# Kernel optimization log

Measured on AMD Instinct MI355X. Metric: run time of the kernel, lower is better.

Reference implementation:

```python
import jax, jax.numpy as jnp
import numpy as np

B, N, C = 1, 768, 384
H, P = 12, 4
DP = 128  # dim_pair
HP3 = H * P * 3  # 144


def linear(x, W, b):
    # torch nn.Linear: y = x @ W.T + b, W shape (out, in)
    return jnp.einsum('...i,oi->...o', x, W) + b


def setup_inputs() -> dict:
    key = jax.random.key(0)
    ks = jax.random.split(key, 24)
    w = lambda k, *s: jax.random.normal(k, s, jnp.float32) * 0.02
    inp = {
        'single': jax.random.normal(ks[0], (B, N, C), jnp.float32),
        'pair': jax.random.normal(ks[1], (B, N, N, DP), jnp.float32),
        'rot': jax.random.normal(ks[2], (B, N, 3, 3), jnp.float32),
        'trans': jax.random.normal(ks[3], (B, N, 3), jnp.float32),
        'Wq': w(ks[4], C, C), 'bq': jnp.zeros((C,), jnp.float32),
        'Wk': w(ks[5], C, C), 'bk': jnp.zeros((C,), jnp.float32),
        'Wv': w(ks[6], C, C), 'bv': jnp.zeros((C,), jnp.float32),
        'Wpb': w(ks[7], H, DP), 'bpb': jnp.zeros((H,), jnp.float32),
        'Wqp': w(ks[8], HP3, C), 'bqp': jnp.zeros((HP3,), jnp.float32),
        'Wkp': w(ks[9], HP3, C), 'bkp': jnp.zeros((HP3,), jnp.float32),
        'Wvp': w(ks[10], HP3, C), 'bvp': jnp.zeros((HP3,), jnp.float32),
        'Wo': w(ks[11], C, C), 'bo': jnp.zeros((C,), jnp.float32),
        'Wpo': w(ks[12], C, HP3), 'bpo': jnp.zeros((C,), jnp.float32),
        'ln_w': jnp.ones((C,), jnp.float32), 'ln_b': jnp.zeros((C,), jnp.float32),
    }
    return inp


def reference(single, pair, rot, trans, Wq, bq, Wk, bk, Wv, bv, Wpb, bpb,
              Wqp, bqp, Wkp, bkp, Wvp, bvp, Wo, bo, Wpo, bpo, ln_w, ln_b):
    Ch = C // H
    scale = Ch ** -0.5
    q = linear(single, Wq, bq).reshape(B, N, H, Ch)
    k = linear(single, Wk, bk).reshape(B, N, H, Ch)
    v = linear(single, Wv, bv).reshape(B, N, H, Ch)
    pair_bias = jnp.transpose(linear(pair, Wpb, bpb), (0, 3, 1, 2))  # (B,H,N,N)

    q_pts = linear(single, Wqp, bqp).reshape(B, N, H, P, 3)
    k_pts = linear(single, Wkp, bkp).reshape(B, N, H, P, 3)
    v_pts = linear(single, Wvp, bvp).reshape(B, N, H, P, 3)
    t = trans[:, :, None, None, :]  # (B,N,1,1,3)
    # rotate local points into global frame: p @ R + t
    q_g = jnp.einsum('bnhpd,bnde->bnhpe', q_pts, rot) + t
    k_g = jnp.einsum('bnhpd,bnde->bnhpe', k_pts, rot) + t
    v_g = jnp.einsum('bnhpd,bnde->bnhpe', v_pts, rot) + t

    q2 = jnp.sum(q_g ** 2, axis=(3, 4))  # (B,N,H)
    k2 = jnp.sum(k_g ** 2, axis=(3, 4))
    qk = jnp.einsum('bnhpd,bmhpd->bhnm', q_g, k_g)
    q2h = jnp.transpose(q2, (0, 2, 1))  # (B,H,N)
    k2h = jnp.transpose(k2, (0, 2, 1))
    point_logits = -0.5 * (q2h[..., :, None] + k2h[..., None, :] - 2.0 * qk) * scale
    scalar_logits = jnp.einsum('bnhc,bmhc->bhnm', q, k) * scale
    attn = jax.nn.softmax(scalar_logits + pair_bias + point_logits, axis=-1)

    weighted_scalar = jnp.einsum('bhnm,bmhc->bnhc', attn, v).reshape(B, N, C)
    weighted_points = jnp.einsum('bhnm,bmhpd->bnhpd', attn, v_g).reshape(B, N, HP3)
    point_proj = linear(weighted_points, Wpo, bpo)
    out = linear(weighted_scalar + point_proj, Wo, bo)

    x = single + out
    mu = jnp.mean(x, axis=-1, keepdims=True)
    var = jnp.mean((x - mu) ** 2, axis=-1, keepdims=True)
    return (x - mu) / jnp.sqrt(var + 1e-5) * ln_w + ln_b
```

## Files before the change

### kernel.cpp

```cpp
#include <hip/hip_runtime.h>
#include <math.h>

#define NRES 768
#define CDIM 384
#define HEADS 12
#define SCALE 0.17677669529663687f

typedef _Float16 f16;
typedef _Float16 __attribute__((ext_vector_type(8))) f16x8;
typedef float __attribute__((ext_vector_type(4))) f32x4;

__device__ __forceinline__ f16x8 ldcvt8(const float* __restrict__ p) {
  float4 a = *(const float4*)p;
  float4 b = *(const float4*)(p + 4);
  f16x8 r = {(f16)a.x, (f16)a.y, (f16)a.z, (f16)a.w,
             (f16)b.x, (f16)b.y, (f16)b.z, (f16)b.w};
  return r;
}

__device__ __forceinline__ void mfma_step(f16 (*As)[64], f16 (*Bs)[64],
                                          int w, int lg, int lr, f32x4* acc) {
#pragma unroll
  for (int ks = 0; ks < 2; ++ks) {
    f16x8 af = *(const f16x8*)&As[w * 16 + lr][((ks * 4 + lg) ^ (lr & 7)) * 8];
#pragma unroll
    for (int c = 0; c < 4; ++c) {
      f16x8 bf = *(const f16x8*)&Bs[c * 16 + lr][((ks * 4 + lg) ^ (lr & 7)) * 8];
      acc[c] = __builtin_amdgcn_mfma_f32_16x16x32_f16(af, bf, acc[c], 0, 0, 0);
    }
  }
}

__global__ __launch_bounds__(512) void k1_mega(
    const float* __restrict__ pair, const float* __restrict__ Wpb, const float* __restrict__ bpb,
    const float* __restrict__ single,
    const float* __restrict__ Wq, const float* __restrict__ Wk, const float* __restrict__ Wv,
    const float* __restrict__ Wqp, const float* __restrict__ Wkp, const float* __restrict__ Wvp,
    const float* __restrict__ bq, const float* __restrict__ bk, const float* __restrict__ bv,
    const float* __restrict__ bqp, const float* __restrict__ bkp, const float* __restrict__ bvp,
    const float* __restrict__ Wpo, const float* __restrict__ bpo, const float* __restrict__ Wo,
    f16* __restrict__ biasb, f16* __restrict__ Wcomb, f16* __restrict__ S16) {
  __shared__ f16 smem[12 * 1160];
  const int bid = blockIdx.x;
  const int t = threadIdx.x;
  const int w = t >> 6, l = t & 63;
  const int lg = l >> 4, lr = l & 15;
  const f16 z0 = (f16)0.f;

  if (bid < 576) {
    f16* bias_l = smem;
    const int mblk = bid % 12;
    const int q0 = (bid / 12) * 16;
    const int m0 = mblk * 64;
    f16x8 bfr[4];
#pragma unroll
    for (int ks = 0; ks < 4; ++ks)
#pragma unroll
      for (int j = 0; j < 8; ++j)
        bfr[ks][j] = (f16)((lr < HEADS) ? Wpb[lr * 128 + ks * 32 + lg * 8 + j] : 0.f);
    const float bh = (lr < HEADS) ? bpb[lr] : 0.f;
#pragma unroll
    for (int g8 = 0; g8 < 8; ++g8) {
      const int g = w * 8 + g8;
      const int rowf = g * 16 + lr;
      const int nf = rowf >> 6, mf = rowf & 63;
      const float* ap = pair + (((size_t)(q0 + nf)) * NRES + (m0 + mf)) * 128 + lg * 8;
      f32x4 acc = {0.f, 0.f, 0.f, 0.f};
#pragma unroll
      for (int ks = 0; ks < 4; ++ks) {
        float4 a0 = *(const float4*)(ap + ks * 32);
        float4 a1 = *(const float4*)(ap + ks * 32 + 4);
        f16x8 af = {(f16)a0.x, (f16)a0.y, (f16)a0.z, (f16)a0.w,
                    (f16)a1.x, (f16)a1.y, (f16)a1.z, (f16)a1.w};
        acc = __builtin_amdgcn_mfma_f32_16x16x32_f16(af, bfr[ks], acc, 0, 0, 0);
      }
      if (lr < HEADS) {
#pragma unroll
        for (int r = 0; r < 4; ++r) {
          int rowo = g * 16 + lg * 4 + r;
          bias_l[lr * 1160 + (rowo >> 6) * 72 + (rowo & 63)] = (f16)(acc[r] + bh);
        }
      }
    }
    __syncthreads();
    for (int i = t; i < 12 * 16 * 8; i += 512) {
      int h = i >> 7;
      int rem = i & 127;
      int row = rem >> 3, c8 = rem & 7;
      *(f16x8*)(biasb + (size_t)h * (NRES * NRES) + (size_t)(q0 + row) * NRES + m0 + c8 * 8) =
          *(const f16x8*)&smem[h * 1160 + row * 72 + c8 * 8];
    }
    return;
  }

  f16 (*As)[64] = (f16(*)[64])smem;
  f16 (*Bs)[64] = (f16(*)[64])(smem + 4096);
  const int wm = w & 3, wn = w >> 2;
  f32x4 acc[2] = {{0.f,0.f,0.f,0.f},{0.f,0.f,0.f,0.f}};

  if (bid < 876) {
    const int i = bid - 576;
    const int bm = (i / 25) * 64, bn = (i % 25) * 64;
    for (int k0 = 0; k0 < 384; k0 += 64) {
      __syncthreads();
      {
        int row = t >> 3, k8 = t & 7;
        int sw = (k8 ^ (row & 7)) * 8;
        *(f16x8*)&As[row][sw] = ldcvt8(single + (size_t)(bm + row) * 384 + k0 + k8 * 8);
        int o = bn + row;
        const float* bsrc;
        if (o < 384)       bsrc = Wq  + (size_t)o * 384;
        else if (o < 768)  bsrc = Wk  + (size_t)(o - 384) * 384;
        else if (o < 1152) bsrc = Wv  + (size_t)(o - 768) * 384;
        else if (o < 1296) bsrc = Wqp + (size_t)(o - 1152) * 384;
        else if (o < 1440) bsrc = Wkp + (size_t)(o - 1296) * 384;
        else if (o < 1584) bsrc = Wvp + (size_t)(o - 1440) * 384;
        else               bsrc = nullptr;
        f16x8 vb8 = {z0, z0, z0, z0, z0, z0, z0, z0};
        if (bsrc) vb8 = ldcvt8(bsrc + k0 + k8 * 8);
        *(f16x8*)&Bs[row][sw] = vb8;
      }
      __syncthreads();
#pragma unroll
      for (int ks = 0; ks < 2; ++ks) {
        f16x8 af = *(const f16x8*)&As[wm * 16 + lr][((ks * 4 + lg) ^ (lr & 7)) * 8];
#pragma unroll
        for (int j = 0; j < 2; ++j) {
          f16x8 bf = *(const f16x8*)&Bs[(wn * 2 + j) * 16 + lr][((ks * 4 + lg) ^ (lr & 7)) * 8];
          acc[j] = __builtin_amdgcn_mfma_f32_16x16x32_f16(af, bf, acc[j], 0, 0, 0);
        }
      }
    }
#pragma unroll
    for (int j = 0; j < 2; ++j) {
      int col = bn + (wn * 2 + j) * 16 + lr;
      if (col >= 1584) continue;
      float bb;
      if (col < 384)       bb = bq[col];
      else if (col < 768)  bb = bk[col - 384];
      else if (col < 1152) bb = bv[col - 768];
      else if (col < 1296) bb = bqp[col - 1152];
      else if (col < 1440) bb = bkp[col - 1296];
      else                 bb = bvp[col - 1440];
#pragma unroll
      for (int r = 0; r < 4; ++r) {
        int row = bm + wm * 16 + lg * 4 + r;
        S16[(size_t)row * 1584 + col] = (f16)(acc[j][r] + bb);
      }
    }
  } else {
    const int i = bid - 876;
    const int bm = (i / 3) * 64, bn = (i % 3) * 64;
    for (int k0 = 0; k0 < 384; k0 += 64) {
      __syncthreads();
      {
        int row = t >> 3, k8 = t & 7;
        int sw = (k8 ^ (row & 7)) * 8;
        *(f16x8*)&As[row][sw] = ldcvt8(Wo + (size_t)(bm + row) * 384 + k0 + k8 * 8);
        int pr = bn + row;
        f16x8 vb8 = {z0, z0, z0, z0, z0, z0, z0, z0};
        if (pr < 144) {
#pragma unroll
          for (int j = 0; j < 8; ++j) vb8[j] = (f16)Wpo[(size_t)(k0 + k8 * 8 + j) * 144 + pr];
        } else if (pr == 144) {
#pragma unroll
          for (int j = 0; j < 8; ++j) vb8[j] = (f16)bpo[k0 + k8 * 8 + j];
        }
        *(f16x8*)&Bs[row][sw] = vb8;
      }
      __syncthreads();
#pragma unroll
      for (int ks = 0; ks < 2; ++ks) {
        f16x8 af = *(const f16x8*)&As[wm * 16 + lr][((ks * 4 + lg) ^ (lr & 7)) * 8];
#pragma unroll
        for (int j = 0; j < 2; ++j) {
          f16x8 bf = *(const f16x8*)&Bs[(wn * 2 + j) * 16 + lr][((ks * 4 + lg) ^ (lr & 7)) * 8];
          acc[j] = __builtin_amdgcn_mfma_f32_16x16x32_f16(af, bf, acc[j], 0, 0, 0);
        }
      }
    }
#pragma unroll
    for (int j = 0; j < 2; ++j) {
      int col = bn + (wn * 2 + j) * 16 + lr;
      if (col >= 192) continue;
#pragma unroll
      for (int r = 0; r < 4; ++r)
        Wcomb[(size_t)(bm + wm * 16 + lg * 4 + r) * 192 + col] = (f16)acc[j][r];
    }
  }
}

__global__ __launch_bounds__(256) void final_gemm(
    const f16* __restrict__ attn_cat, const float* __restrict__ Wo,
    const f16* __restrict__ Wcomb, const float* __restrict__ bo,
    const float* __restrict__ single, float* __restrict__ xb) {
  __shared__ f16 As[64][64];
  __shared__ f16 Bs[64][64];
  const int t = threadIdx.x;
  const int w = t >> 6, l = t & 63;
  const int lg = l >> 4, lr = l & 15;
  const int bm = blockIdx.y * 64, bn = blockIdx.x * 64;
  f32x4 acc[4] = {{0.f,0.f,0.f,0.f},{0.f,0.f,0.f,0.f},{0.f,0.f,0.f,0.f},{0.f,0.f,0.f,0.f}};
  for (int k0 = 0; k0 < 576; k0 += 64) {
    __syncthreads();
#pragma unroll
    for (int cc = 0; cc < 2; ++cc) {
      int c = t + cc * 256;
      int row = c >> 3, k8 = c & 7;
      int sw = (k8 ^ (row & 7)) * 8;
      *(f16x8*)&As[row][sw] = *(const f16x8*)(attn_cat + (size_t)(bm + row) * 576 + k0 + k8 * 8);
      f16x8 vb8;
      if (k0 < 384) vb8 = ldcvt8(Wo + (size_t)(bn + row) * 384 + k0 + k8 * 8);
      else          vb8 = *(const f16x8*)(Wcomb + (size_t)(bn + row) * 192 + (k0 - 384) + k8 * 8);
      *(f16x8*)&Bs[row][sw] = vb8;
    }
    __syncthreads();
    mfma_step(As, Bs, w, lg, lr, acc);
  }
#pragma unroll
  for (int c = 0; c < 4; ++c) {
    int col = bn + c * 16 + lr;
    float bb = bo[col];
#pragma unroll
    for (int r = 0; r < 4; ++r) {
      int row = bm + w * 16 + lg * 4 + r;
      xb[(size_t)row * 384 + col] = acc[c][r] + bb + single[(size_t)row * 384 + col];
    }
  }
}

__global__ __launch_bounds__(64) void rot_feats3(
    const f16* __restrict__ S16, const float* __restrict__ rot, const float* __restrict__ trans,
    f16* __restrict__ qf, f16* __restrict__ kf, f16* __restrict__ vfT) {
  const int n = blockIdx.x * 64 + threadIdx.x;
  const int h = blockIdx.y;
  const f16* Sr = S16 + (size_t)n * 1584;
  float R[9], T[3];
#pragma unroll
  for (int i = 0; i < 9; ++i) R[i] = rot[n * 9 + i];
#pragma unroll
  for (int i = 0; i < 3; ++i) T[i] = trans[n * 3 + i];
  f16 qh[64], kh[64];
  f16x8 qv4[4], kv4[4], vv4[4];
#pragma unroll
  for (int j = 0; j < 4; ++j) {
    qv4[j] = *(const f16x8*)(Sr + h * 32 + j * 8);
    kv4[j] = *(const f16x8*)(Sr + 384 + h * 32 + j * 8);
    vv4[j] = *(const f16x8*)(Sr + 768 + h * 32 + j * 8);
  }
#pragma unroll
  for (int c = 0; c < 32; ++c) {
    qh[c] = (f16)(SCALE * (float)qv4[c >> 3][c & 7]);
    vfT[((size_t)(h * 48 + c)) * NRES + n] = vv4[c >> 3][c & 7];
  }
#pragma unroll
  for (int j = 0; j < 4; ++j) *(f16x8*)&kh[j * 8] = kv4[j];
  float qp[12], kp[12], vp[12];
#pragma unroll
  for (int e = 0; e < 12; ++e) {
    qp[e] = (float)Sr[1152 + h * 12 + e];
    kp[e] = (float)Sr[1296 + h * 12 + e];
    vp[e] = (float)Sr[1440 + h * 12 + e];
  }
  float q2 = 0.f, k2 = 0.f;
#pragma unroll
  for (int p = 0; p < 4; ++p) {
#pragma unroll
    for (int e = 0; e < 3; ++e) {
      float qg = qp[p*3+0] * R[e] + qp[p*3+1] * R[3+e] + qp[p*3+2] * R[6+e] + T[e];
      float kg = kp[p*3+0] * R[e] + kp[p*3+1] * R[3+e] + kp[p*3+2] * R[6+e] + T[e];
      float vg = vp[p*3+0] * R[e] + vp[p*3+1] * R[3+e] + vp[p*3+2] * R[6+e] + T[e];
      qh[32 + p*3 + e] = (f16)(SCALE * qg); q2 += qg * qg;
      kh[32 + p*3 + e] = (f16)kg;           k2 += kg * kg;
      vfT[((size_t)(h * 48 + 32 + p*3 + e)) * NRES + n] = (f16)vg;
    }
  }
  qh[44] = (f16)(-0.5f * SCALE * q2); qh[45] = (f16)1.f;
  kh[44] = (f16)1.f;                  kh[45] = (f16)(-0.5f * SCALE * k2);
#pragma unroll
  for (int c = 46; c < 64; ++c) { qh[c] = (f16)0.f; kh[c] = (f16)0.f; }
#pragma unroll
  for (int c = 44; c < 48; ++c) vfT[((size_t)(h * 48 + c)) * NRES + n] = (f16)0.f;
  f16* qo = qf + ((size_t)(h * NRES + n)) * 64;
  f16* ko = kf + ((size_t)(h * NRES + n)) * 64;
#pragma unroll
  for (int j = 0; j < 8; ++j) {
    *(f16x8*)&qo[j * 8] = *(const f16x8*)&qh[j * 8];
    *(f16x8*)&ko[j * 8] = *(const f16x8*)&kh[j * 8];
  }
}

__global__ __launch_bounds__(512) void attn_full(
    const f16* __restrict__ biasb,
    const f16* __restrict__ qf, const f16* __restrict__ kf, const f16* __restrict__ vfT,
    f16* __restrict__ attn_cat) {
  __shared__ f16 bias_l[16 * 776];
  __shared__ float redO[8][16][48];
  __shared__ float redD[8][16];
  const int t = threadIdx.x;
  const int w = t >> 6, l = t & 63;
  const int lg = l >> 4, lr = l & 15;
  const int h = blockIdx.x;
  const int q0 = blockIdx.y * 16;

  {
    const f16* src = biasb + (size_t)h * (NRES * NRES) + (size_t)q0 * NRES;
    for (int i = t; i < 16 * 96; i += 512) {
      int row = i / 96, c8 = i % 96;
      *(f16x8*)&bias_l[row * 776 + c8 * 8] = *(const f16x8*)(src + (size_t)row * NRES + c8 * 8);
    }
  }
  const f16* qrow = qf + ((size_t)(h * NRES + q0 + lr)) * 64;
  f16x8 qa0 = *(const f16x8*)(qrow + lg * 8);
  f16x8 qa1 = *(const f16x8*)(qrow + 32 + lg * 8);
  __syncthreads();

  float den[4] = {0.f, 0.f, 0.f, 0.f};
#pragma unroll
  for (int mc2 = 0; mc2 < 6; ++mc2) {
    const int mcol = w * 96 + mc2 * 16;
    const f16* krow = kf + ((size_t)(h * NRES + mcol + lr)) * 64;
    f16x8 kb0 = *(const f16x8*)(krow + lg * 8);
    f16x8 kb1 = *(const f16x8*)(krow + 32 + lg * 8);
    f32x4 s = {0.f, 0.f, 0.f, 0.f};
    s = __builtin_amdgcn_mfma_f32_16x16x32_f16(qa0, kb0, s, 0, 0, 0);
    s = __builtin_amdgcn_mfma_f32_16x16x32_f16(qa1, kb1, s, 0, 0, 0);
#pragma unroll
    for (int r = 0; r < 4; ++r) {
      const int pidx = (lg * 4 + r) * 776 + mcol + lr;
      float b = (float)bias_l[pidx];
      float e = __expf(s[r] + b);
      den[r] += e;
      bias_l[pidx] = (f16)e;
    }
  }
#pragma unroll
  for (int r = 0; r < 4; ++r) {
    float d = den[r];
    d += __shfl_xor(d, 1); d += __shfl_xor(d, 2);
    d += __shfl_xor(d, 4); d += __shfl_xor(d, 8);
    if (lr == 0) redD[w][lg * 4 + r] = d;
  }
  f32x4 a0 = {0.f,0.f,0.f,0.f}, a1 = {0.f,0.f,0.f,0.f}, a2 = {0.f,0.f,0.f,0.f};
#pragma unroll
  for (int ks = 0; ks < 3; ++ks) {
    const int mbase = w * 96 + ks * 32;
    f16x8 pa = *(const f16x8*)&bias_l[lr * 776 + mbase + lg * 8];
    const f16* vbase = vfT + ((size_t)(h * 48 + lr)) * NRES + mbase + lg * 8;
    f16x8 vb0 = *(const f16x8*)(vbase);
    f16x8 vb1 = *(const f16x8*)(vbase + 16 * NRES);
    f16x8 vb2 = *(const f16x8*)(vbase + 32 * NRES);
    a0 = __builtin_amdgcn_mfma_f32_16x16x32_f16(pa, vb0, a0, 0, 0, 0);
    a1 = __builtin_amdgcn_mfma_f32_16x16x32_f16(pa, vb1, a1, 0, 0, 0);
    a2 = __builtin_amdgcn_mfma_f32_16x16x32_f16(pa, vb2, a2, 0, 0, 0);
  }
#pragma unroll
  for (int r = 0; r < 4; ++r) {
    redO[w][lg * 4 + r][lr]      = a0[r];
    redO[w][lg * 4 + r][16 + lr] = a1[r];
    redO[w][lg * 4 + r][32 + lr] = a2[r];
  }
  __syncthreads();
  for (int o = t; o < 16 * 48; o += 512) {
    int q = o / 48, c = o % 48;
    float num = 0.f, ds = 0.f;
#pragma unroll
    for (int ww = 0; ww < 8; ++ww) { num += redO[ww][q][c]; ds += redD[ww][q]; }
    float val = num / ds;
    int n = q0 + q;
    if (c < 32)      attn_cat[(size_t)n * 576 + h * 32 + c] = (f16)val;
    else if (c < 44) attn_cat[(size_t)n * 576 + 384 + h * 12 + (c - 32)] = (f16)val;
  }
  if (h == 0) {
    for (int o = t; o < 16 * 48; o += 512) {
      int q = o / 48, c = o % 48;
      attn_cat[(size_t)(q0 + q) * 576 + 528 + c] = (f16)(c == 0 ? 1.f : 0.f);
    }
  }
}

__global__ __launch_bounds__(64) void ln_kernel(
    const float* __restrict__ x, const float* __restrict__ w, const float* __restrict__ b,
    float* __restrict__ out) {
  int n = blockIdx.x;
  int l = threadIdx.x;
  const float* xr = x + (size_t)n * CDIM;
  float v[6];
  float s = 0.f;
#pragma unroll
  for (int i = 0; i < 6; ++i) { v[i] = xr[l + 64 * i]; s += v[i]; }
#pragma unroll
  for (int o = 32; o; o >>= 1) s += __shfl_xor(s, o);
  float mu = s * (1.f / 384.f);
  float vs = 0.f;
#pragma unroll
  for (int i = 0; i < 6; ++i) { float d = v[i] - mu; vs += d * d; }
#pragma unroll
  for (int o = 32; o; o >>= 1) vs += __shfl_xor(vs, o);
  float rstd = rsqrtf(vs * (1.f / 384.f) + 1e-5f);
  float* orow = out + (size_t)n * CDIM;
#pragma unroll
  for (int i = 0; i < 6; ++i) {
    int c = l + 64 * i;
    orow[c] = (v[i] - mu) * rstd * w[c] + b[c];
  }
}

extern "C" void kernel_launch(void* const* d_in, const int* in_sizes, int n_in,
                              void* d_out, int out_size, void* d_ws, size_t ws_size,
                              hipStream_t stream) {
  const float* single = (const float*)d_in[0];
  const float* pair   = (const float*)d_in[1];
  const float* rot    = (const float*)d_in[2];
  const float* trans  = (const float*)d_in[3];
  const float* Wq  = (const float*)d_in[4];
  const float* bq  = (const float*)d_in[5];
  const float* Wk  = (const float*)d_in[6];
  const float* bk  = (const float*)d_in[7];
  const float* Wv  = (const float*)d_in[8];
  const float* bv  = (const float*)d_in[9];
  const float* Wpb = (const float*)d_in[10];
  const float* bpb = (const float*)d_in[11];
  const float* Wqp = (const float*)d_in[12];
  const float* bqp = (const float*)d_in[13];
  const float* Wkp = (const float*)d_in[14];
  const float* bkp = (const float*)d_in[15];
  const float* Wvp = (const float*)d_in[16];
  const float* bvp = (const float*)d_in[17];
  const float* Wo  = (const float*)d_in[18];
  const float* bo  = (const float*)d_in[19];
  const float* Wpo = (const float*)d_in[20];
  const float* bpo = (const float*)d_in[21];
  const float* lnw = (const float*)d_in[22];
  const float* lnb = (const float*)d_in[23];

  float* ws = (float*)d_ws;
  f16* S16      = (f16*)ws; ws += 768 * 1584 / 2;
  f16* Wcomb    = (f16*)ws; ws += 384 * 192 / 2;
  f16* biasb    = (f16*)ws; ws += 12 * 768 * 768 / 2;
  f16* qf       = (f16*)ws; ws += 12 * 768 * 64 / 2;
  f16* kf       = (f16*)ws; ws += 12 * 768 * 64 / 2;
  f16* vfT      = (f16*)ws; ws += 12 * 48 * 768 / 2;
  f16* attn_cat = (f16*)ws; ws += 768 * 576 / 2;
  float* xb     = ws;       ws += 768 * 384;

  k1_mega<<<894, 512, 0, stream>>>(pair, Wpb, bpb, single,
                                   Wq, Wk, Wv, Wqp, Wkp, Wvp,
                                   bq, bk, bv, bqp, bkp, bvp,
                                   Wpo, bpo, Wo, biasb, Wcomb, S16);
  rot_feats3<<<dim3(12, 12), 64, 0, stream>>>(S16, rot, trans, qf, kf, vfT);
  attn_full<<<dim3(12, 48), 512, 0, stream>>>(biasb, qf, kf, vfT, attn_cat);
  final_gemm<<<dim3(6, 12), 256, 0, stream>>>(attn_cat, Wo, Wcomb, bo, single, xb);
  ln_kernel<<<768, 64, 0, stream>>>(xb, lnw, lnb, (float*)d_out);
}
```

Baseline: 114.2 us.

## Stream pair tiles via global_load_lds double buffering in the bias projection

The pair-bias projection now loads pair data with asynchronous global-to-LDS DMA (global_load_lds) into a per-wave double buffer, with a rotated swizzle so the later LDS reads avoid bank conflicts. Explicit vmcnt waits keep two chunks in flight while the MFMA for the current chunk runs. This replaces the direct float4 global loads into registers and aims to hide memory latency on the dominant pair stream. It enlarges the shared memory allocation, which can lower occupancy, and the hand-written waitcnt ordering is fragile.

```diff
diff --git a/kernel.cpp b/kernel.cpp
--- a/kernel.cpp
+++ b/kernel.cpp
@@ -40,7 +40,7 @@
     const float* __restrict__ bqp, const float* __restrict__ bkp, const float* __restrict__ bvp,
     const float* __restrict__ Wpo, const float* __restrict__ bpo, const float* __restrict__ Wo,
     f16* __restrict__ biasb, f16* __restrict__ Wcomb, f16* __restrict__ S16) {
-  __shared__ f16 smem[12 * 1160];
+  __shared__ f16 smem[30304];
   const int bid = blockIdx.x;
   const int t = threadIdx.x;
   const int w = t >> 6, l = t & 63;
@@ -49,9 +49,12 @@
 
   if (bid < 576) {
     f16* bias_l = smem;
+    f16* dmaw = smem + 13920 + w * 2048;
+    const float* bpf = (const float*)dmaw;
     const int mblk = bid % 12;
     const int q0 = (bid / 12) * 16;
     const int m0 = mblk * 64;
+
     f16x8 bfr[4];
 #pragma unroll
     for (int ks = 0; ks < 4; ++ks)
@@ -59,25 +62,49 @@
       for (int j = 0; j < 8; ++j)
         bfr[ks][j] = (f16)((lr < HEADS) ? Wpb[lr * 128 + ks * 32 + lg * 8 + j] : 0.f);
     const float bh = (lr < HEADS) ? bpb[lr] : 0.f;
+
+    const int pos0 = l >> 3;
+    const int j7 = l & 7;
+
+    auto issue = [&](int c) {
+      const int g8 = c >> 2, ks = c & 3, buf = c & 1;
+#pragma unroll
+      for (int ii = 0; ii < 2; ++ii) {
+        const int pos = ii * 8 + pos0;
+        const int rowf = w * 128 + g8 * 16 + pos;
+        const float* src = pair
+            + (((size_t)(q0 + (rowf >> 6))) * NRES + (m0 + (rowf & 63))) * 128
+            + ks * 32 + (((j7 - pos) & 7) << 2);
+        __builtin_amdgcn_global_load_lds(
+            (const __attribute__((address_space(1))) unsigned int*)src,
+            (__attribute__((address_space(3))) unsigned int*)(dmaw + buf * 1024 + ii * 512),
+            16, 0, 0);
+      }
+    };
+
+    issue(0); issue(1);
+    const int s0 = (lg * 8 + lr * 4) & 31;
+    const int s1 = (s0 + 4) & 31;
 #pragma unroll
     for (int g8 = 0; g8 < 8; ++g8) {
-      const int g = w * 8 + g8;
-      const int rowf = g * 16 + lr;
-      const int nf = rowf >> 6, mf = rowf & 63;
-      const float* ap = pair + (((size_t)(q0 + nf)) * NRES + (m0 + mf)) * 128 + lg * 8;
       f32x4 acc = {0.f, 0.f, 0.f, 0.f};
 #pragma unroll
       for (int ks = 0; ks < 4; ++ks) {
-        float4 a0 = *(const float4*)(ap + ks * 32);
-        float4 a1 = *(const float4*)(ap + ks * 32 + 4);
-        f16x8 af = {(f16)a0.x, (f16)a0.y, (f16)a0.z, (f16)a0.w,
-                    (f16)a1.x, (f16)a1.y, (f16)a1.z, (f16)a1.w};
+        const int c = g8 * 4 + ks;
+        if (c < 31) asm volatile("s_waitcnt vmcnt(2)" ::: "memory");
+        else        asm volatile("s_waitcnt vmcnt(0)" ::: "memory");
+        const float* bp = bpf + (c & 1) * 512;
+        float4 x0 = *(const float4*)(bp + lr * 32 + s0);
+        float4 x1 = *(const float4*)(bp + lr * 32 + s1);
+        f16x8 af = {(f16)x0.x, (f16)x0.y, (f16)x0.z, (f16)x0.w,
+                    (f16)x1.x, (f16)x1.y, (f16)x1.z, (f16)x1.w};
         acc = __builtin_amdgcn_mfma_f32_16x16x32_f16(af, bfr[ks], acc, 0, 0, 0);
+        if (c + 2 < 32) issue(c + 2);
       }
       if (lr < HEADS) {
 #pragma unroll
         for (int r = 0; r < 4; ++r) {
-          int rowo = g * 16 + lg * 4 + r;
+          int rowo = (w * 8 + g8) * 16 + lg * 4 + r;
           bias_l[lr * 1160 + (rowo >> 6) * 72 + (rowo & 63)] = (f16)(acc[r] + bh);
         }
       }
```

Result: slower. 124.5 us (+9.0%).
